# Kernel optimization log

Measured on AMD Instinct MI355X. Metric: run time of the kernel, lower is better.

Reference implementation:

```python
import jax, jax.numpy as jnp
import numpy as np

GRID_H = 64
GRID_W = 64


def make_grid(h, w):
    # torch.meshgrid([arange(h), arange(w)], indexing='xy') -> shape (w, h);
    # grid[i, j] = (j + 0.5, i + 0.5). With h == w == 64 this is square.
    gx, gy = jnp.meshgrid(jnp.arange(h, dtype=jnp.float32),
                          jnp.arange(w, dtype=jnp.float32), indexing='xy')
    return jnp.stack([gx, gy], axis=-1) + 0.5  # (w, h, 2)


def setup_inputs() -> dict:
    key = jax.random.key(0)
    k1, k2 = jax.random.split(key)
    x = jax.random.normal(k1, (4, 128, 64, 64), dtype=jnp.float32)
    y = jax.random.normal(k2, (4, 128, 64, 64), dtype=jnp.float32)
    return {"x": x, "y": y}


def reference(x, y):
    b, c, hx, wx = x.shape
    _, _, hy, wy = y.shape
    scale = c ** (-0.5)
    grids = make_grid(GRID_H, GRID_W)[:hy, :wy].reshape(-1, 2)  # (hy*wy, 2)

    x_ = x.reshape(b, c, hx * wx)
    y_ = y.reshape(b, c, hy * wy)
    # (b, q, k) attention over all key pixels
    attn = jax.nn.softmax(jnp.einsum('bcq,bck->bqk', x_, y_) * scale, axis=-1)
    uv = jnp.einsum('bqk,kt->bqt', attn, grids)  # (b, hx*wx, 2)
    uv = uv.reshape(b, hx, wx, 2)
    # normalize to [-1, 1]
    norm = jnp.asarray([wy, hy], dtype=uv.dtype)
    uv = uv / norm * 2.0 - 1.0
    return uv
```

## Files before the change

kernel.cpp:

```cpp
#include <hip/hip_runtime.h>
#include <math.h>

typedef __attribute__((ext_vector_type(8))) _Float16 f16x8;
typedef __attribute__((ext_vector_type(4))) float f32x4;

#define NPIX 4096
#define C_DIM 128
#define SCALE2 0.12752064638518208f

#if __has_builtin(__builtin_amdgcn_exp2f)
#define EXP2(x) __builtin_amdgcn_exp2f(x)
#else
#define EXP2(x) exp2f(x)
#endif

#define WS_NEED ((size_t)4 << 20)

__global__ __launch_bounds__(256) void conv_y(const float* __restrict__ y,
                                              char* __restrict__ ws)
{
    __shared__ float T[32][132];
    const int wg  = blockIdx.x;
    const int xcd = wg & 7;
    const int b   = xcd >> 1;
    const int sl  = ((xcd & 1) << 6) | (wg >> 3);
    const int k0  = sl * 32;
    const int t   = threadIdx.x;

    {
        const int c = t >> 1, half = t & 1;
        const float* srow = y + ((size_t)b * C_DIM + c) * NPIX + k0 + half * 16;
        float4 rv[4];
        #pragma unroll
        for (int u = 0; u < 4; ++u) rv[u] = *(const float4*)(srow + u * 4);
        #pragma unroll
        for (int u = 0; u < 4; ++u) {
            T[half * 16 + u * 4 + 0][c] = rv[u].x;
            T[half * 16 + u * 4 + 1][c] = rv[u].y;
            T[half * 16 + u * 4 + 2][c] = rv[u].z;
            T[half * 16 + u * 4 + 3][c] = rv[u].w;
        }
    }
    __syncthreads();

    char* panel = ws + (size_t)b * (NPIX * 256);
    const int k = t >> 3, g2 = t & 7;
    f16x8 v0, v1;
    #pragma unroll
    for (int m = 0; m < 8; ++m) {
        v0[m] = (_Float16)T[k][g2 * 16 + m];
        v1[m] = (_Float16)T[k][g2 * 16 + 8 + m];
    }
    const int key = k0 + k, s = key & 7;
    char* drow = panel + (size_t)key * 256;
    *(f16x8*)(drow + (((2 * g2)     ^ s) << 4)) = v0;
    *(f16x8*)(drow + (((2 * g2 + 1) ^ s) << 4)) = v1;
}

__global__ __launch_bounds__(512, 4) void uv_main(const char* __restrict__ ws,
                                                  const float* __restrict__ x,
                                                  float* __restrict__ out)
{
    __shared__ __align__(16) char Ys[2][32768];
    __shared__ float red[8][32][3];

    const int t = threadIdx.x, w = t >> 6, l = t & 63;
    const int n16 = l & 15, quad = l >> 4;
    const int wg  = blockIdx.x;
    const int xcd = wg & 7;
    const int b   = xcd >> 1;
    const int qt  = ((xcd & 1) << 6) | (wg >> 3);
    const int q0  = qt * 32;

    const char* panel = ws + (size_t)b * (NPIX * 256);

    int soff[4];
    #pragma unroll
    for (int i = 0; i < 4; ++i) soff[i] = (w * 16 + i * 4) * 256 + l * 16;

    #pragma unroll
    for (int i = 0; i < 4; ++i)
        __builtin_amdgcn_global_load_lds(
            (const __attribute__((address_space(1))) void*)(panel + soff[i]),
            (__attribute__((address_space(3))) void*)(&Ys[0][soff[i]]), 16, 0, 0);

    f16x8 bx[4][2];
    {
        const float* xq = x + (size_t)b * C_DIM * NPIX + q0 + n16;
        #pragma unroll
        for (int cc = 0; cc < 4; ++cc)
            #pragma unroll
            for (int qg = 0; qg < 2; ++qg) {
                f16x8 hh;
                #pragma unroll
                for (int j = 0; j < 8; ++j)
                    hh[j] = (_Float16)(xq[(size_t)(cc * 32 + quad * 8 + j) * NPIX + qg * 16] * SCALE2);
                bx[cc][qg] = hh;
            }
    }

    const int arow = w * 16 + n16;
    int aoff[4];
    #pragma unroll
    for (int cc = 0; cc < 4; ++cc)
        aoff[cc] = arow * 256 + (((cc * 4 + quad) ^ (n16 & 7)) << 4);

    float gxv[4];
    #pragma unroll
    for (int r = 0; r < 4; ++r) gxv[r] = (float)((w & 3) * 16 + quad * 4 + r) + 0.5f;
    const float gyw = (float)(w >> 2) + 0.5f;
    float den[2] = {0.f, 0.f}, nu[2] = {0.f, 0.f}, nv[2] = {0.f, 0.f};

    #pragma unroll 1
    for (int kt = 0; kt < 32; ++kt) {
        char* cur = Ys[kt & 1];

        if (kt < 31) {
            const char* gt = panel + (size_t)(kt + 1) * 32768;
            char* nb = Ys[(kt + 1) & 1];
            #pragma unroll
            for (int i = 0; i < 4; ++i)
                __builtin_amdgcn_global_load_lds(
                    (const __attribute__((address_space(1))) void*)(gt + soff[i]),
                    (__attribute__((address_space(3))) void*)(&nb[soff[i]]), 16, 0, 0);
            __builtin_amdgcn_s_waitcnt(0x0F74);
        } else {
            __builtin_amdgcn_s_waitcnt(0x0F70);
        }

        f32x4 acc[2];
        #pragma unroll
        for (int qg = 0; qg < 2; ++qg) acc[qg] = (f32x4){0.f, 0.f, 0.f, 0.f};

        #pragma unroll
        for (int cc = 0; cc < 4; ++cc) {
            const f16x8 A = *(const f16x8*)(cur + aoff[cc]);
            #pragma unroll
            for (int qg = 0; qg < 2; ++qg)
                acc[qg] = __builtin_amdgcn_mfma_f32_16x16x32_f16(A, bx[cc][qg], acc[qg], 0, 0, 0);
        }

        const float gy = 2.0f * (float)kt + gyw;
        #pragma unroll
        for (int qg = 0; qg < 2; ++qg) {
            float ps = 0.f, pc = 0.f;
            #pragma unroll
            for (int r = 0; r < 4; ++r) {
                const float p = EXP2(acc[qg][r]);
                ps += p;
                pc += p * gxv[r];
            }
            den[qg] += ps;
            nu[qg]  += pc;
            nv[qg]  += gy * ps;
        }
    }

    #pragma unroll
    for (int qg = 0; qg < 2; ++qg) {
        #pragma unroll
        for (int mk = 16; mk <= 32; mk <<= 1) {
            den[qg] += __shfl_xor(den[qg], mk);
            nu[qg]  += __shfl_xor(nu[qg],  mk);
            nv[qg]  += __shfl_xor(nv[qg],  mk);
        }
    }
    if (quad == 0) {
        #pragma unroll
        for (int qg = 0; qg < 2; ++qg) {
            red[w][qg * 16 + n16][0] = den[qg];
            red[w][qg * 16 + n16][1] = nu[qg];
            red[w][qg * 16 + n16][2] = nv[qg];
        }
    }
    __syncthreads();
    if (t < 32) {
        float d = 0.f, u = 0.f, v = 0.f;
        #pragma unroll
        for (int ww = 0; ww < 8; ++ww) {
            d += red[ww][t][0];
            u += red[ww][t][1];
            v += red[ww][t][2];
        }
        const float inv = 1.0f / d;
        *(float2*)(out + ((size_t)b * NPIX + q0 + t) * 2) =
            make_float2(u * inv * 0.03125f - 1.0f, v * inv * 0.03125f - 1.0f);
    }
}

__global__ __launch_bounds__(256, 2) void uv_attn_kernel(
    const float* __restrict__ x, const float* __restrict__ y, float* __restrict__ out)
{
    __shared__ float Xs[C_DIM][32];
    __shared__ float Ysf[64][128];
    const float SCALE = 0.08838834764831845f;
    const int tid = threadIdx.x;
    const int wgid = blockIdx.x;
    const int xcd = wgid & 7;
    const int b = xcd & 3;
    const int q0 = (((xcd >> 2) << 6) | (wgid >> 3)) * 32;
    const float* xb = x + (size_t)b * C_DIM * NPIX + q0;
    {
        const int cr = tid >> 3;
        const int cc = (tid & 7) << 2;
        #pragma unroll
        for (int i = 0; i < 4; ++i) {
            float4 v = *(const float4*)(xb + (size_t)(cr + (i << 5)) * NPIX + cc);
            v.x *= SCALE; v.y *= SCALE; v.z *= SCALE; v.w *= SCALE;
            *(float4*)(&Xs[cr + (i << 5)][cc]) = v;
        }
    }
    const int rg = tid >> 4;
    const int lane16 = tid & 15;
    const int r0 = rg << 1;
    const int col0 = lane16 << 3;
    float gxv[8];
    #pragma unroll
    for (int j2 = 0; j2 < 8; ++j2) gxv[j2] = (float)((col0 & 63) + j2) + 0.5f;
    const float gyb = (float)(lane16 >> 3) + 0.5f;
    float m_run[2] = {-INFINITY, -INFINITY};
    float den[2] = {0.f, 0.f}, nu[2] = {0.f, 0.f}, nv[2] = {0.f, 0.f};
    const int yr = tid >> 5;
    const int yc = (tid & 31) << 2;
    const float* ybase = y + (size_t)b * C_DIM * NPIX;
    for (int kt = 0; kt < 32; ++kt) {
        float S[2][8];
        #pragma unroll
        for (int r = 0; r < 2; ++r)
            #pragma unroll
            for (int j2 = 0; j2 < 8; ++j2) S[r][j2] = 0.f;
        #pragma unroll
        for (int cb = 0; cb < 2; ++cb) {
            __syncthreads();
            const float* yt = ybase + (size_t)(cb << 6) * NPIX + kt * 128;
            #pragma unroll
            for (int i = 0; i < 8; ++i)
                *(float4*)(&Ysf[yr + (i << 3)][yc]) =
                    *(const float4*)(yt + (size_t)(yr + (i << 3)) * NPIX + yc);
            __syncthreads();
            const int cbase = cb << 6;
            #pragma unroll 16
            for (int c = 0; c < 64; ++c) {
                const float2 xa = *(const float2*)(&Xs[cbase + c][r0]);
                const float4 ya = *(const float4*)(&Ysf[c][col0]);
                const float4 yb4 = *(const float4*)(&Ysf[c][col0 + 4]);
                S[0][0] += xa.x * ya.x;  S[0][1] += xa.x * ya.y;
                S[0][2] += xa.x * ya.z;  S[0][3] += xa.x * ya.w;
                S[0][4] += xa.x * yb4.x; S[0][5] += xa.x * yb4.y;
                S[0][6] += xa.x * yb4.z; S[0][7] += xa.x * yb4.w;
                S[1][0] += xa.y * ya.x;  S[1][1] += xa.y * ya.y;
                S[1][2] += xa.y * ya.z;  S[1][3] += xa.y * ya.w;
                S[1][4] += xa.y * yb4.x; S[1][5] += xa.y * yb4.y;
                S[1][6] += xa.y * yb4.z; S[1][7] += xa.y * yb4.w;
            }
        }
        const float gy = gyb + 2.0f * (float)kt;
        #pragma unroll
        for (int r = 0; r < 2; ++r) {
            float tmax = S[r][0];
            #pragma unroll
            for (int j2 = 1; j2 < 8; ++j2) tmax = fmaxf(tmax, S[r][j2]);
            #pragma unroll
            for (int mk = 8; mk >= 1; mk >>= 1) tmax = fmaxf(tmax, __shfl_xor(tmax, mk, 16));
            const float mnew = fmaxf(m_run[r], tmax);
            const float alpha = __expf(m_run[r] - mnew);
            m_run[r] = mnew;
            float psum = 0.f, pu = 0.f;
            #pragma unroll
            for (int j2 = 0; j2 < 8; ++j2) {
                const float p = __expf(S[r][j2] - mnew);
                psum += p; pu += p * gxv[j2];
            }
            den[r] = den[r] * alpha + psum;
            nu[r] = nu[r] * alpha + pu;
            nv[r] = nv[r] * alpha + gy * psum;
        }
    }
    #pragma unroll
    for (int r = 0; r < 2; ++r)
        #pragma unroll
        for (int mk = 8; mk >= 1; mk >>= 1) {
            den[r] += __shfl_xor(den[r], mk, 16);
            nu[r] += __shfl_xor(nu[r], mk, 16);
            nv[r] += __shfl_xor(nv[r], mk, 16);
        }
    if (lane16 == 0) {
        #pragma unroll
        for (int r = 0; r < 2; ++r) {
            const float inv = 1.0f / den[r];
            const int q = q0 + r0 + r;
            *(float2*)(out + ((size_t)b * NPIX + q) * 2) =
                make_float2(nu[r] * inv * 0.03125f - 1.0f, nv[r] * inv * 0.03125f - 1.0f);
        }
    }
}

extern "C" void kernel_launch(void* const* d_in, const int* in_sizes, int n_in,
                              void* d_out, int out_size, void* d_ws, size_t ws_size,
                              hipStream_t stream) {
    const float* x = (const float*)d_in[0];
    const float* y = (const float*)d_in[1];
    float* out = (float*)d_out;
    if (ws_size >= WS_NEED) {
        hipLaunchKernelGGL(conv_y, dim3(512), dim3(256), 0, stream, y, (char*)d_ws);
        hipLaunchKernelGGL(uv_main, dim3(512), dim3(512), 0, stream,
                           (const char*)d_ws, x, out);
    } else {
        hipLaunchKernelGGL(uv_attn_kernel, dim3(512), dim3(256), 0, stream, x, y, out);
    }
}
```

Baseline: 95.80 us.

## Double uv_main query and key tiles with 1024-thread blocks

Each uv_main block now covers 64 queries instead of 32 and streams 256-key tiles of 64 KB instead of 128-key tiles. It runs 16 waves over 256 blocks, and each wave computes four query groups against every loaded A fragment. This halves how many times the fp16 Y panel is fetched from global memory and written to LDS per query. The costs are a larger register footprint from bx[4][4] plus four sets of accumulators, more LDS per block (about 140 KB, so one block per CU), and a 16-wave reduction at the end.

```diff
diff --git a/kernel.cpp b/kernel.cpp
--- a/kernel.cpp
+++ b/kernel.cpp
@@ -57,20 +57,20 @@
     *(f16x8*)(drow + (((2 * g2 + 1) ^ s) << 4)) = v1;
 }
 
-__global__ __launch_bounds__(512, 4) void uv_main(const char* __restrict__ ws,
-                                                  const float* __restrict__ x,
-                                                  float* __restrict__ out)
+__global__ __launch_bounds__(1024) void uv_main(const char* __restrict__ ws,
+                                                const float* __restrict__ x,
+                                                float* __restrict__ out)
 {
-    __shared__ __align__(16) char Ys[2][32768];
-    __shared__ float red[8][32][3];
+    __shared__ __align__(16) char Ys[2][65536];
+    __shared__ float red[16][64][3];
 
     const int t = threadIdx.x, w = t >> 6, l = t & 63;
     const int n16 = l & 15, quad = l >> 4;
     const int wg  = blockIdx.x;
     const int xcd = wg & 7;
     const int b   = xcd >> 1;
-    const int qt  = ((xcd & 1) << 6) | (wg >> 3);
-    const int q0  = qt * 32;
+    const int qt  = ((xcd & 1) << 5) | (wg >> 3);
+    const int q0  = qt * 64;
 
     const char* panel = ws + (size_t)b * (NPIX * 256);
 
@@ -84,13 +84,13 @@
             (const __attribute__((address_space(1))) void*)(panel + soff[i]),
             (__attribute__((address_space(3))) void*)(&Ys[0][soff[i]]), 16, 0, 0);
 
-    f16x8 bx[4][2];
+    f16x8 bx[4][4];
     {
         const float* xq = x + (size_t)b * C_DIM * NPIX + q0 + n16;
         #pragma unroll
         for (int cc = 0; cc < 4; ++cc)
             #pragma unroll
-            for (int qg = 0; qg < 2; ++qg) {
+            for (int qg = 0; qg < 4; ++qg) {
                 f16x8 hh;
                 #pragma unroll
                 for (int j = 0; j < 8; ++j)
@@ -109,14 +109,14 @@
     #pragma unroll
     for (int r = 0; r < 4; ++r) gxv[r] = (float)((w & 3) * 16 + quad * 4 + r) + 0.5f;
     const float gyw = (float)(w >> 2) + 0.5f;
-    float den[2] = {0.f, 0.f}, nu[2] = {0.f, 0.f}, nv[2] = {0.f, 0.f};
+    float den[4] = {0.f, 0.f, 0.f, 0.f}, nu[4] = {0.f, 0.f, 0.f, 0.f}, nv[4] = {0.f, 0.f, 0.f, 0.f};
 
     #pragma unroll 1
-    for (int kt = 0; kt < 32; ++kt) {
+    for (int kt = 0; kt < 16; ++kt) {
         char* cur = Ys[kt & 1];
 
-        if (kt < 31) {
-            const char* gt = panel + (size_t)(kt + 1) * 32768;
+        if (kt < 15) {
+            const char* gt = panel + (size_t)(kt + 1) * 65536;
             char* nb = Ys[(kt + 1) & 1];
             #pragma unroll
             for (int i = 0; i < 4; ++i)
@@ -128,36 +128,52 @@
             __builtin_amdgcn_s_waitcnt(0x0F70);
         }
 
-        f32x4 acc[2];
-        #pragma unroll
-        for (int qg = 0; qg < 2; ++qg) acc[qg] = (f32x4){0.f, 0.f, 0.f, 0.f};
-
-        #pragma unroll
-        for (int cc = 0; cc < 4; ++cc) {
-            const f16x8 A = *(const f16x8*)(cur + aoff[cc]);
-            #pragma unroll
-            for (int qg = 0; qg < 2; ++qg)
-                acc[qg] = __builtin_amdgcn_mfma_f32_16x16x32_f16(A, bx[cc][qg], acc[qg], 0, 0, 0);
-        }
-
-        const float gy = 2.0f * (float)kt + gyw;
-        #pragma unroll
-        for (int qg = 0; qg < 2; ++qg) {
-            float ps = 0.f, pc = 0.f;
+        const float gy = 4.0f * (float)kt + gyw;
+
+        {
+            f32x4 acc0 = (f32x4){0.f, 0.f, 0.f, 0.f};
+            f32x4 acc1 = (f32x4){0.f, 0.f, 0.f, 0.f};
+            #pragma unroll
+            for (int cc = 0; cc < 4; ++cc) {
+                const f16x8 A = *(const f16x8*)(cur + aoff[cc]);
+                acc0 = __builtin_amdgcn_mfma_f32_16x16x32_f16(A, bx[cc][0], acc0, 0, 0, 0);
+                acc1 = __builtin_amdgcn_mfma_f32_16x16x32_f16(A, bx[cc][1], acc1, 0, 0, 0);
+            }
+            float ps0 = 0.f, pc0 = 0.f, ps1 = 0.f, pc1 = 0.f;
             #pragma unroll
             for (int r = 0; r < 4; ++r) {
-                const float p = EXP2(acc[qg][r]);
-                ps += p;
-                pc += p * gxv[r];
-            }
-            den[qg] += ps;
-            nu[qg]  += pc;
-            nv[qg]  += gy * ps;
-        }
-    }
-
-    #pragma unroll
-    for (int qg = 0; qg < 2; ++qg) {
+                const float p0 = EXP2(acc0[r]);
+                const float p1 = EXP2(acc1[r]);
+                ps0 += p0; pc0 += p0 * gxv[r];
+                ps1 += p1; pc1 += p1 * gxv[r];
+            }
+            den[0] += ps0; nu[0] += pc0; nv[0] += gy * ps0;
+            den[1] += ps1; nu[1] += pc1; nv[1] += gy * ps1;
+        }
+        {
+            f32x4 acc0 = (f32x4){0.f, 0.f, 0.f, 0.f};
+            f32x4 acc1 = (f32x4){0.f, 0.f, 0.f, 0.f};
+            #pragma unroll
+            for (int cc = 0; cc < 4; ++cc) {
+                const f16x8 A = *(const f16x8*)(cur + aoff[cc]);
+                acc0 = __builtin_amdgcn_mfma_f32_16x16x32_f16(A, bx[cc][2], acc0, 0, 0, 0);
+                acc1 = __builtin_amdgcn_mfma_f32_16x16x32_f16(A, bx[cc][3], acc1, 0, 0, 0);
+            }
+            float ps0 = 0.f, pc0 = 0.f, ps1 = 0.f, pc1 = 0.f;
+            #pragma unroll
+            for (int r = 0; r < 4; ++r) {
+                const float p0 = EXP2(acc0[r]);
+                const float p1 = EXP2(acc1[r]);
+                ps0 += p0; pc0 += p0 * gxv[r];
+                ps1 += p1; pc1 += p1 * gxv[r];
+            }
+            den[2] += ps0; nu[2] += pc0; nv[2] += gy * ps0;
+            den[3] += ps1; nu[3] += pc1; nv[3] += gy * ps1;
+        }
+    }
+
+    #pragma unroll
+    for (int qg = 0; qg < 4; ++qg) {
         #pragma unroll
         for (int mk = 16; mk <= 32; mk <<= 1) {
             den[qg] += __shfl_xor(den[qg], mk);
@@ -167,17 +183,17 @@
     }
     if (quad == 0) {
         #pragma unroll
-        for (int qg = 0; qg < 2; ++qg) {
+        for (int qg = 0; qg < 4; ++qg) {
             red[w][qg * 16 + n16][0] = den[qg];
             red[w][qg * 16 + n16][1] = nu[qg];
             red[w][qg * 16 + n16][2] = nv[qg];
         }
     }
     __syncthreads();
-    if (t < 32) {
+    if (t < 64) {
         float d = 0.f, u = 0.f, v = 0.f;
         #pragma unroll
-        for (int ww = 0; ww < 8; ++ww) {
+        for (int ww = 0; ww < 16; ++ww) {
             d += red[ww][t][0];
             u += red[ww][t][1];
             v += red[ww][t][2];
@@ -303,7 +319,7 @@
     float* out = (float*)d_out;
     if (ws_size >= WS_NEED) {
         hipLaunchKernelGGL(conv_y, dim3(512), dim3(256), 0, stream, y, (char*)d_ws);
-        hipLaunchKernelGGL(uv_main, dim3(512), dim3(512), 0, stream,
+        hipLaunchKernelGGL(uv_main, dim3(256), dim3(1024), 0, stream,
                            (const char*)d_ws, x, out);
     } else {
         hipLaunchKernelGGL(uv_attn_kernel, dim3(512), dim3(256), 0, stream, x, y, out);
```

New measurement: 93.11 us. 2.8% less time.
